# Kernel optimization log

Hardware: AMD Instinct MI355X
Metric: run time of the kernel (lower is better)

Reference implementation:

```python
import jax, jax.numpy as jnp
import numpy as np

B, S, H, NH = 2, 2048, 1024, 16
DH = H // NH


def setup_inputs() -> dict:
    key = jax.random.key(0)
    ks = jax.random.split(key, 8)
    scale = 0.02
    return {
        "q": jax.random.normal(ks[0], (B, S, H), dtype=jnp.float32),
        "attention_mask": jax.random.uniform(ks[1], (B, 1, 1, S), dtype=jnp.float32),
        "Wq": jax.random.normal(ks[2], (H, H), dtype=jnp.float32) * scale,
        "bq": jnp.zeros((H,), dtype=jnp.float32),
        "Wk": jax.random.normal(ks[3], (H, H), dtype=jnp.float32) * scale,
        "bk": jnp.zeros((H,), dtype=jnp.float32),
        "Wv": jax.random.normal(ks[4], (H, H), dtype=jnp.float32) * scale,
        "bv": jnp.zeros((H,), dtype=jnp.float32),
    }


def _split_heads(x):
    # [B, S, H] -> [B, NH, S, DH]
    b, s, _ = x.shape
    return x.reshape(b, s, NH, DH).transpose(0, 2, 1, 3)


def reference(q, attention_mask, Wq, bq, Wk, bk, Wv, bv):
    # self-attention: k = v = q
    query = _split_heads(q @ Wq + bq)  # [B, NH, S, DH]
    key = _split_heads(q @ Wk + bk)
    value = _split_heads(q @ Wv + bv)

    scores = jnp.einsum("bhqd,bhkd->bhqk", query, key) / jnp.sqrt(
        jnp.asarray(DH, dtype=query.dtype)
    )
    scores = scores * attention_mask  # multiplicative mask (non-standard)
    attn = jax.nn.softmax(scores, axis=-1)  # dropout off (training=False)
    ctx = jnp.einsum("bhqk,bhkd->bhqd", attn, value)  # [B, NH, S, DH]
    ctx = ctx.transpose(0, 2, 1, 3).reshape(q.shape[0], -1, NH * DH)
    return ctx, attn
```

## Files before the change

kernel.cpp:

```cpp
#include <hip/hip_runtime.h>
#include <hip/hip_bf16.h>

#define B_ 2
#define S_ 2048
#define H_ 1024
#define NH_ 16
#define DH_ 64
#define M_ (B_*S_)
#define N3_ (3*H_)
#define K_ H_

typedef __attribute__((ext_vector_type(8))) short bf16x8;
typedef __attribute__((ext_vector_type(4))) short bf16x4;
typedef __attribute__((ext_vector_type(4))) float f32x4;

__device__ __forceinline__ short f2bf(float f) {
  union { float fv; unsigned u; } v; v.fv = f;
  return (short)((v.u + 0x7FFFu + ((v.u >> 16) & 1u)) >> 16);
}
__device__ __forceinline__ float bf2f(short s) {
  union { unsigned u; float fv; } v; v.u = ((unsigned)(unsigned short)s) << 16;
  return v.fv;
}

#define MFMA16(a,b,c) __builtin_amdgcn_mfma_f32_16x16x32_bf16((a),(b),(c),0,0,0)

__global__ __launch_bounds__(256) void convert_q(const float* __restrict__ q,
                                                 short* __restrict__ qb) {
  int i = blockIdx.x * blockDim.x + threadIdx.x;
  f32x4 v = ((const f32x4*)q)[i];
  bf16x4 o = { f2bf(v[0]), f2bf(v[1]), f2bf(v[2]), f2bf(v[3]) };
  ((bf16x4*)qb)[i] = o;
}

__global__ __launch_bounds__(256) void transpose_w(const float* __restrict__ Wq,
                                                   const float* __restrict__ Wk,
                                                   const float* __restrict__ Wv,
                                                   short* __restrict__ Wt) {
  __shared__ float tile[32][33];
  int w = blockIdx.z;
  const float* W = (w == 0) ? Wq : ((w == 1) ? Wk : Wv);
  int n0 = blockIdx.x * 32, k0 = blockIdx.y * 32;
  int tx = threadIdx.x, ty = threadIdx.y;
  for (int i = 0; i < 4; i++)
    tile[ty + 8*i][tx] = W[(size_t)(k0 + ty + 8*i) * H_ + n0 + tx];
  __syncthreads();
  for (int i = 0; i < 4; i++)
    Wt[(size_t)w * H_ * H_ + (size_t)(n0 + ty + 8*i) * H_ + k0 + tx] =
        f2bf(tile[tx][ty + 8*i]);
}

__global__ __launch_bounds__(256) void qkv_gemm(
    const short* __restrict__ qb,
    const short* __restrict__ Wt,
    const float* __restrict__ bq, const float* __restrict__ bk,
    const float* __restrict__ bv,
    short* __restrict__ Qws, short* __restrict__ Kws, short* __restrict__ VT) {
  __shared__ short Wtile[128 * 32];
  __shared__ short Qtile[128 * 32];

  int bidx = blockIdx.x;
  int mt = bidx & 31, nt = bidx >> 5;
  int t = threadIdx.x;
  int wave = t >> 6, lane = t & 63;
  int g = lane >> 4, l15 = lane & 15;
  int nh = (wave & 1) * 64, mh = (wave >> 1) * 64;
  int mblk = mt * 128, nblk = nt * 128;

  int srow = t >> 2, ssub = t & 3;
  const short* wsrc = Wt + (size_t)(nblk + srow) * K_ + ssub * 8;
  const short* qsrc = qb + (size_t)(mblk + srow) * K_ + ssub * 8;
  short* wdst0 = Wtile + wave * 512;
  short* qdst0 = Qtile + wave * 512;

  f32x4 acc[4][4];
#pragma unroll
  for (int i = 0; i < 4; i++)
#pragma unroll
    for (int j = 0; j < 4; j++) acc[i][j] = (f32x4){0.f,0.f,0.f,0.f};

  for (int k0 = 0; k0 < K_; k0 += 32) {
    __builtin_amdgcn_global_load_lds(wsrc + k0,         wdst0,         16, 0, 0);
    __builtin_amdgcn_global_load_lds(wsrc + 64*K_ + k0, wdst0 + 64*32, 16, 0, 0);
    __builtin_amdgcn_global_load_lds(qsrc + k0,         qdst0,         16, 0, 0);
    __builtin_amdgcn_global_load_lds(qsrc + 64*K_ + k0, qdst0 + 64*32, 16, 0, 0);
    __syncthreads();
    bf16x8 af[4], bfr[4];
#pragma unroll
    for (int tn = 0; tn < 4; tn++)
      af[tn] = *(const bf16x8*)(Wtile + (nh + tn*16 + l15) * 32 + g * 8);
#pragma unroll
    for (int tm = 0; tm < 4; tm++)
      bfr[tm] = *(const bf16x8*)(Qtile + (mh + tm*16 + l15) * 32 + g * 8);
#pragma unroll
    for (int tn = 0; tn < 4; tn++)
#pragma unroll
      for (int tm = 0; tm < 4; tm++)
        acc[tn][tm] = MFMA16(af[tn], bfr[tm], acc[tn][tm]);
    __syncthreads();
  }

  int which = nblk >> 10;
  int cbase = nblk & 1023;
  const float* bias = (which == 0) ? bq : ((which == 1) ? bk : bv);

#pragma unroll
  for (int tm = 0; tm < 4; tm++) {
    int m = mblk + mh + tm*16 + l15;
    int b = m >> 11, s = m & 2047;
#pragma unroll
    for (int tn = 0; tn < 4; tn++) {
      int c = cbase + nh + tn*16 + 4*g;
      int head = c >> 6, d0 = c & 63;
      f32x4 bia = *(const f32x4*)(bias + c);
      short o[4];
#pragma unroll
      for (int r = 0; r < 4; r++) o[r] = f2bf(acc[tn][tm][r] + bia[r]);
      if (which == 2) {
        short* base = VT + ((size_t)(b*NH_ + head) * DH_ + d0) * S_ + s;
#pragma unroll
        for (int r = 0; r < 4; r++) base[(size_t)r * S_] = o[r];
      } else {
        short* dst = ((which == 0) ? Qws : Kws)
                   + ((size_t)(b*NH_ + head) * S_ + s) * DH_ + d0;
        bf16x4 o4 = {o[0], o[1], o[2], o[3]};
        *(bf16x4*)dst = o4;
      }
    }
  }
}

#define STG_K(bufi, kt) do { \
    __builtin_amdgcn_global_load_lds(kSw + (size_t)(kt)*4096,        &Kb[bufi][w*2048],      16, 0, 0); \
    __builtin_amdgcn_global_load_lds(kSw + (size_t)(kt)*4096 + 512,  &Kb[bufi][w*2048+512],  16, 0, 0); \
    __builtin_amdgcn_global_load_lds(kSw + (size_t)(kt)*4096 + 1024, &Kb[bufi][w*2048+1024], 16, 0, 0); \
    __builtin_amdgcn_global_load_lds(kSw + (size_t)(kt)*4096 + 1536, &Kb[bufi][w*2048+1536], 16, 0, 0); \
  } while (0)

__global__ __launch_bounds__(128, 2) void attn_lcalc(
    const short* __restrict__ Qws, const short* __restrict__ Kws,
    const float* __restrict__ mask, float* __restrict__ Linv) {
  __shared__ short Kb[2][4096];
  int bid = blockIdx.x;
  int bh = bid >> 5, qt = bid & 31;
  int tid = threadIdx.x;
  int w = tid >> 6, lane = tid & 63;
  int g = lane >> 4, l15 = lane & 15;
  int lr = lane >> 3, l7 = lane & 7;
  int b = bh >> 4;
  int qbase = qt * 64 + w * 32;

  const short* Kh = Kws + (size_t)bh * S_ * DH_;
  const float* mk = mask + b * S_;
  int sw = 8 * (l15 & 7);
  int swc = 8 * (l7 ^ lr);
  const short* kSw = Kh + (size_t)(w*32 + lr) * DH_ + swc;

  const short* qr0 = Qws + (size_t)bh * S_ * DH_ + (size_t)(qbase + l15) * DH_;
  const short* qr1 = qr0 + 16 * DH_;
  bf16x8 q0a = *(const bf16x8*)(qr0 + 8*g), q0b = *(const bf16x8*)(qr0 + 32 + 8*g);
  bf16x8 q1a = *(const bf16x8*)(qr1 + 8*g), q1b = *(const bf16x8*)(qr1 + 32 + 8*g);

  f32x4 ls0 = (f32x4){0.f,0.f,0.f,0.f}, ls1 = (f32x4){0.f,0.f,0.f,0.f};
  STG_K(0, 0);
  __syncthreads();
  int cur = 0;
  for (int kt = 0; kt < 32; kt++) {
    if (kt + 1 < 32) STG_K(cur ^ 1, kt + 1);
    const short* Kt = Kb[cur];
#pragma unroll
    for (int s0i = 0; s0i < 4; s0i++) {
      int s0 = s0i * 16;
      const short* kp = Kt + (s0 + l15) * 64;
      bf16x8 kf0 = *(const bf16x8*)(kp + ((8*g) ^ sw));
      bf16x8 kf1 = *(const bf16x8*)(kp + ((32 + 8*g) ^ sw));
      f32x4 a0 = (f32x4){0.f,0.f,0.f,0.f}, a1 = (f32x4){0.f,0.f,0.f,0.f};
      a0 = MFMA16(kf0, q0a, a0); a0 = MFMA16(kf1, q0b, a0);
      a1 = MFMA16(kf0, q1a, a1); a1 = MFMA16(kf1, q1b, a1);
      f32x4 mv = *(const f32x4*)(mk + kt*64 + s0 + 4*g);
#pragma unroll
      for (int r = 0; r < 4; r++) {
        ls0[r] += __expf(a0[r] * 0.125f * mv[r]);
        ls1[r] += __expf(a1[r] * 0.125f * mv[r]);
      }
    }
    __syncthreads();
    cur ^= 1;
  }
  float l0 = ls0[0]+ls0[1]+ls0[2]+ls0[3];
  float l1 = ls1[0]+ls1[1]+ls1[2]+ls1[3];
  l0 += __shfl_xor(l0, 16); l0 += __shfl_xor(l0, 32);
  l1 += __shfl_xor(l1, 16); l1 += __shfl_xor(l1, 32);
  if (lane < 16) {
    Linv[(size_t)bh * S_ + qbase + lane]      = 1.f / l0;
    Linv[(size_t)bh * S_ + qbase + 16 + lane] = 1.f / l1;
  }
}

#define STG_K4(bufi, kt) do { \
    __builtin_amdgcn_global_load_lds(kS4 + (size_t)(kt)*4096,          &Kb[bufi][w*1024],      16, 0, 0); \
    __builtin_amdgcn_global_load_lds(kS4 + (size_t)(kt)*4096 + 8*DH_,  &Kb[bufi][w*1024+512],  16, 0, 0); \
  } while (0)
#define STG_V4(bufi, kt) do { \
    __builtin_amdgcn_global_load_lds(vS4 + (size_t)(kt)*64,            &Vb[bufi][w*1024],      16, 0, 0); \
    __builtin_amdgcn_global_load_lds(vS4 + (size_t)(kt)*64 + 8*(size_t)S_, &Vb[bufi][w*1024+512], 16, 0, 0); \
  } while (0)

__global__ __launch_bounds__(256, 2) void attn_main(
    const short* __restrict__ Qws, const short* __restrict__ Kws,
    const short* __restrict__ VT, const float* __restrict__ mask,
    const float* __restrict__ Linv,
    float* __restrict__ ctx, float* __restrict__ attn) {
  __shared__ short Kb[2][4096];
  __shared__ short Vb[2][4096];
  __shared__ short Pb[64 * 256];
  int bid = blockIdx.x;
  int bh = bid >> 5, qt = bid & 31;
  int tid = threadIdx.x;
  int w = tid >> 6, lane = tid & 63;
  int g = lane >> 4, l15 = lane & 15;
  int lhi = lane >> 3, l7 = lane & 7;
  int b = bh >> 4, h = bh & 15;
  int qbase = qt * 64 + w * 16;

  const short* Kh = Kws + (size_t)bh * S_ * DH_;
  const short* Vh = VT  + (size_t)bh * DH_ * S_;
  const float* mk = mask + b * S_;
  int sw = 8 * (l15 & 7);
  int swc = 8 * (l7 ^ lhi);
  const short* kS4 = Kh + (size_t)(w*16 + lhi) * DH_ + swc;
  const short* vS4 = Vh + (size_t)(w*16 + lhi) * S_  + swc;

  const short* qr0 = Qws + (size_t)bh * S_ * DH_ + (size_t)(qbase + l15) * DH_;
  bf16x8 q0a = *(const bf16x8*)(qr0 + 8*g), q0b = *(const bf16x8*)(qr0 + 32 + 8*g);
  float linv = Linv[(size_t)bh * S_ + qbase + l15];

  f32x4 oc[4];
#pragma unroll
  for (int tv = 0; tv < 4; tv++) oc[tv] = (f32x4){0.f,0.f,0.f,0.f};

  int prow = w*16 + l15;
  float* ablk = attn + ((size_t)bh * S_ + qt*64) * (size_t)S_;

  STG_K4(0, 0); STG_V4(0, 0);
  __syncthreads();
  int cur = 0;
  for (int st = 0; st < 8; st++) {
#pragma unroll
    for (int j = 0; j < 4; j++) {
      int kt = st*4 + j;
      if (kt + 1 < 32) { STG_K4(cur ^ 1, kt + 1); STG_V4(cur ^ 1, kt + 1); }
      const short* Kt = Kb[cur];
      const short* Vt = Vb[cur];
#pragma unroll
      for (int khi = 0; khi < 2; khi++) {
        int kh = khi * 32;
        bf16x8 pa;
#pragma unroll
        for (int half = 0; half < 2; half++) {
          int s0 = kh + half * 16;
          const short* kp = Kt + (s0 + l15) * 64;
          bf16x8 kf0 = *(const bf16x8*)(kp + ((8*g) ^ sw));
          bf16x8 kf1 = *(const bf16x8*)(kp + ((32 + 8*g) ^ sw));
          f32x4 a0 = (f32x4){0.f,0.f,0.f,0.f};
          a0 = MFMA16(kf0, q0a, a0); a0 = MFMA16(kf1, q0b, a0);
          f32x4 mv = *(const f32x4*)(mk + kt*64 + s0 + 4*g);
          bf16x4 p4;
#pragma unroll
          for (int r = 0; r < 4; r++) {
            float p = __expf(a0[r] * 0.125f * mv[r]) * linv;
            short pb = f2bf(p);
            p4[r] = pb;
            pa[half*4 + r] = pb;
          }
          int lk = j*64 + s0 + 4*g;
          int ps = prow*256 + ((lk & 7) | ((((lk >> 3) ^ (prow & 7))) << 3));
          *(bf16x4*)(&Pb[ps]) = p4;
        }
#pragma unroll
        for (int tv = 0; tv < 4; tv++) {
          const short* vp = Vt + (tv*16 + l15) * 64;
          bf16x4 va = *(const bf16x4*)(vp + ((kh + 4*g) ^ sw));
          bf16x4 vb2 = *(const bf16x4*)(vp + ((kh + 16 + 4*g) ^ sw));
          bf16x8 vf = {va[0],va[1],va[2],va[3], vb2[0],vb2[1],vb2[2],vb2[3]};
          oc[tv] = MFMA16(pa, vf, oc[tv]);
        }
      }
      __syncthreads();
      cur ^= 1;
    }
#pragma unroll
    for (int i = 0; i < 16; i++) {
      int row = w*16 + i;
      int lk = 4 * lane;
      int ps = row*256 + ((lk & 7) | ((((lk >> 3) ^ (row & 7))) << 3));
      bf16x4 pv4 = *(const bf16x4*)(&Pb[ps]);
      f32x4 o = { bf2f(pv4[0]), bf2f(pv4[1]), bf2f(pv4[2]), bf2f(pv4[3]) };
      *(f32x4*)(ablk + (size_t)row * S_ + st*256 + lk) = o;
    }
    __syncthreads();
  }

#pragma unroll
  for (int tv = 0; tv < 4; tv++) {
#pragma unroll
    for (int r = 0; r < 4; r++) {
      int q = qbase + 4*g + r;
      ctx[((size_t)b * S_ + q) * H_ + h * DH_ + tv*16 + l15] = oc[tv][r];
    }
  }
}

extern "C" void kernel_launch(void* const* d_in, const int* in_sizes, int n_in,
                              void* d_out, int out_size, void* d_ws, size_t ws_size,
                              hipStream_t stream) {
  const float* q    = (const float*)d_in[0];
  const float* mask = (const float*)d_in[1];
  const float* Wq   = (const float*)d_in[2];
  const float* bq   = (const float*)d_in[3];
  const float* Wk   = (const float*)d_in[4];
  const float* bk   = (const float*)d_in[5];
  const float* Wv   = (const float*)d_in[6];
  const float* bv   = (const float*)d_in[7];

  float* ctx  = (float*)d_out;
  float* attn = ctx + (size_t)B_ * S_ * H_;

  short* qb  = (short*)d_ws;
  short* Wt  = qb  + (size_t)M_ * K_;
  short* Qws = Wt  + (size_t)N3_ * K_;
  short* Kws = Qws + (size_t)B_ * NH_ * S_ * DH_;
  short* VT  = Kws + (size_t)B_ * NH_ * S_ * DH_;
  float* Linv = (float*)(VT + (size_t)B_ * NH_ * S_ * DH_);

  convert_q<<<(M_ * K_) / (256 * 4), 256, 0, stream>>>(q, qb);
  transpose_w<<<dim3(32, 32, 3), dim3(32, 8), 0, stream>>>(Wq, Wk, Wv, Wt);
  qkv_gemm<<<768, 256, 0, stream>>>(qb, Wt, bq, bk, bv, Qws, Kws, VT);
  attn_lcalc<<<1024, 128, 0, stream>>>(Qws, Kws, mask, Linv);
  attn_main<<<1024, 256, 0, stream>>>(Qws, Kws, VT, mask, Linv, ctx, attn);
}
```

Measured before the change: 263.0 us.

## Double-buffer P tile and interleave attn stores with compute, swizzle block order

Replaces the single 256-column P buffer, which was flushed after every four key tiles behind an extra barrier, with two 128-column buffers. The previous buffer is drained to global memory in slices during later key-tile iterations, overlapping the large attn write with the QK/PV MFMA work and removing one barrier per stage. The attn stores become nontemporal, and both kernels remap blockIdx so consecutive blocks spread across heads. This adds index arithmetic and a tail flush, and it changes the L2 locality pattern.

Result: faster. 211.3 us (-19.7%).

```diff
diff --git a/kernel.cpp b/kernel.cpp
--- a/kernel.cpp
+++ b/kernel.cpp
@@ -141,7 +141,8 @@
     const short* __restrict__ Qws, const short* __restrict__ Kws,
     const float* __restrict__ mask, float* __restrict__ Linv) {
   __shared__ short Kb[2][4096];
-  int bid = blockIdx.x;
+  int bid0 = blockIdx.x;
+  int bid = (bid0 & 7) * 128 + (bid0 >> 3);
   int bh = bid >> 5, qt = bid & 31;
   int tid = threadIdx.x;
   int w = tid >> 6, lane = tid & 63;
@@ -213,13 +214,15 @@
     float* __restrict__ ctx, float* __restrict__ attn) {
   __shared__ short Kb[2][4096];
   __shared__ short Vb[2][4096];
-  __shared__ short Pb[64 * 256];
-  int bid = blockIdx.x;
+  __shared__ short Pb[2][64 * 128];
+  int bid0 = blockIdx.x;
+  int bid = (bid0 & 7) * 128 + (bid0 >> 3);
   int bh = bid >> 5, qt = bid & 31;
   int tid = threadIdx.x;
   int w = tid >> 6, lane = tid & 63;
   int g = lane >> 4, l15 = lane & 15;
   int lhi = lane >> 3, l7 = lane & 7;
+  int l31 = lane & 31, lh = lane >> 5;
   int b = bh >> 4, h = bh & 15;
   int qbase = qt * 64 + w * 16;
 
@@ -245,60 +248,74 @@
   STG_K4(0, 0); STG_V4(0, 0);
   __syncthreads();
   int cur = 0;
-  for (int st = 0; st < 8; st++) {
-#pragma unroll
-    for (int j = 0; j < 4; j++) {
-      int kt = st*4 + j;
-      if (kt + 1 < 32) { STG_K4(cur ^ 1, kt + 1); STG_V4(cur ^ 1, kt + 1); }
-      const short* Kt = Kb[cur];
-      const short* Vt = Vb[cur];
-#pragma unroll
-      for (int khi = 0; khi < 2; khi++) {
-        int kh = khi * 32;
-        bf16x8 pa;
-#pragma unroll
-        for (int half = 0; half < 2; half++) {
-          int s0 = kh + half * 16;
-          const short* kp = Kt + (s0 + l15) * 64;
-          bf16x8 kf0 = *(const bf16x8*)(kp + ((8*g) ^ sw));
-          bf16x8 kf1 = *(const bf16x8*)(kp + ((32 + 8*g) ^ sw));
-          f32x4 a0 = (f32x4){0.f,0.f,0.f,0.f};
-          a0 = MFMA16(kf0, q0a, a0); a0 = MFMA16(kf1, q0b, a0);
-          f32x4 mv = *(const f32x4*)(mk + kt*64 + s0 + 4*g);
-          bf16x4 p4;
-#pragma unroll
-          for (int r = 0; r < 4; r++) {
-            float p = __expf(a0[r] * 0.125f * mv[r]) * linv;
-            short pb = f2bf(p);
-            p4[r] = pb;
-            pa[half*4 + r] = pb;
-          }
-          int lk = j*64 + s0 + 4*g;
-          int ps = prow*256 + ((lk & 7) | ((((lk >> 3) ^ (prow & 7))) << 3));
-          *(bf16x4*)(&Pb[ps]) = p4;
+  for (int kt = 0; kt < 32; kt++) {
+    if (kt + 1 < 32) { STG_K4(cur ^ 1, kt + 1); STG_V4(cur ^ 1, kt + 1); }
+    if (kt >= 2) {
+      int pst = (kt >> 1) - 1;
+      const short* Pp = Pb[pst & 1];
+      int rbase = w*16 + 8*(kt & 1);
+#pragma unroll
+      for (int i = 0; i < 4; i++) {
+        int row = rbase + 2*i + lh;
+        int gi2 = l31 ^ ((row & 7) << 2);
+        bf16x4 pv4 = *(const bf16x4*)(&Pp[row*128 + (gi2 << 2)]);
+        f32x4 o = { bf2f(pv4[0]), bf2f(pv4[1]), bf2f(pv4[2]), bf2f(pv4[3]) };
+        __builtin_nontemporal_store(o,
+            (f32x4*)(ablk + (size_t)row * S_ + pst*128 + 4*l31));
+      }
+    }
+    const short* Kt = Kb[cur];
+    const short* Vt = Vb[cur];
+    short* Pcur = Pb[(kt >> 1) & 1];
+#pragma unroll
+    for (int khi = 0; khi < 2; khi++) {
+      int kh = khi * 32;
+      bf16x8 pa;
+#pragma unroll
+      for (int half = 0; half < 2; half++) {
+        int s0 = kh + half * 16;
+        const short* kp = Kt + (s0 + l15) * 64;
+        bf16x8 kf0 = *(const bf16x8*)(kp + ((8*g) ^ sw));
+        bf16x8 kf1 = *(const bf16x8*)(kp + ((32 + 8*g) ^ sw));
+        f32x4 a0 = (f32x4){0.f,0.f,0.f,0.f};
+        a0 = MFMA16(kf0, q0a, a0); a0 = MFMA16(kf1, q0b, a0);
+        f32x4 mv = *(const f32x4*)(mk + kt*64 + s0 + 4*g);
+        bf16x4 p4;
+#pragma unroll
+        for (int r = 0; r < 4; r++) {
+          float p = __expf(a0[r] * 0.125f * mv[r]) * linv;
+          short pb = f2bf(p);
+          p4[r] = pb;
+          pa[half*4 + r] = pb;
         }
-#pragma unroll
-        for (int tv = 0; tv < 4; tv++) {
-          const short* vp = Vt + (tv*16 + l15) * 64;
-          bf16x4 va = *(const bf16x4*)(vp + ((kh + 4*g) ^ sw));
-          bf16x4 vb2 = *(const bf16x4*)(vp + ((kh + 16 + 4*g) ^ sw));
-          bf16x8 vf = {va[0],va[1],va[2],va[3], vb2[0],vb2[1],vb2[2],vb2[3]};
-          oc[tv] = MFMA16(pa, vf, oc[tv]);
-        }
-      }
-      __syncthreads();
-      cur ^= 1;
-    }
-#pragma unroll
-    for (int i = 0; i < 16; i++) {
-      int row = w*16 + i;
-      int lk = 4 * lane;
-      int ps = row*256 + ((lk & 7) | ((((lk >> 3) ^ (row & 7))) << 3));
-      bf16x4 pv4 = *(const bf16x4*)(&Pb[ps]);
+        int lk = (kt & 1)*64 + s0 + 4*g;
+        int gi = (lk >> 2) ^ ((prow & 7) << 2);
+        *(bf16x4*)(&Pcur[prow*128 + (gi << 2)]) = p4;
+      }
+#pragma unroll
+      for (int tv = 0; tv < 4; tv++) {
+        const short* vp = Vt + (tv*16 + l15) * 64;
+        bf16x4 va = *(const bf16x4*)(vp + ((kh + 4*g) ^ sw));
+        bf16x4 vb2 = *(const bf16x4*)(vp + ((kh + 16 + 4*g) ^ sw));
+        bf16x8 vf = {va[0],va[1],va[2],va[3], vb2[0],vb2[1],vb2[2],vb2[3]};
+        oc[tv] = MFMA16(pa, vf, oc[tv]);
+      }
+    }
+    __syncthreads();
+    cur ^= 1;
+  }
+
+  {
+    const short* Pp = Pb[1];
+#pragma unroll
+    for (int i = 0; i < 8; i++) {
+      int row = w*16 + 2*i + lh;
+      int gi2 = l31 ^ ((row & 7) << 2);
+      bf16x4 pv4 = *(const bf16x4*)(&Pp[row*128 + (gi2 << 2)]);
       f32x4 o = { bf2f(pv4[0]), bf2f(pv4[1]), bf2f(pv4[2]), bf2f(pv4[3]) };
-      *(f32x4*)(ablk + (size_t)row * S_ + st*256 + lk) = o;
-    }
-    __syncthreads();
+      __builtin_nontemporal_store(o,
+          (f32x4*)(ablk + (size_t)row * S_ + 15*128 + 4*l31));
+    }
   }
 
 #pragma unroll
```
